# Kernel optimization log

Hardware: AMD Instinct MI355X
Metric: run time of the kernel (lower is better)

The kernel has to match this reference:

```python
import jax, jax.numpy as jnp
import numpy as np

NR_ACTIONS = 64
VEC_SIZE = 512
BATCH = 2048


def setup_inputs() -> dict:
    key = jax.random.key(0)
    k1, k2, k3 = jax.random.split(key, 3)
    v = jax.random.normal(k1, (BATCH, VEC_SIZE), dtype=jnp.float32)
    action = jax.random.randint(k2, (BATCH,), 0, NR_ACTIONS, dtype=jnp.int32)
    # nn.Linear(vec_size, vec_size) default init: U(-1/sqrt(in), 1/sqrt(in))
    bound = 1.0 / np.sqrt(VEC_SIZE)
    weights = jax.random.uniform(
        k3, (NR_ACTIONS, VEC_SIZE, VEC_SIZE), dtype=jnp.float32,
        minval=-bound, maxval=bound)
    return {"v": v, "action": action, "weights": weights}


def reference(v, action, weights):
    # pred[b] = v[b] @ weights[action[b]]  (row-vector times gathered matrix,
    # matching v.unsqueeze(1).bmm(weights.index_select(0, action)).squeeze(1))
    return jnp.einsum('bi,bij->bj', v, weights[action])
```

## Files before the change

kernel.cpp:

```cpp
#include <hip/hip_runtime.h>
#include <hip/hip_bf16.h>

#define NR_ACTIONS 64
#define VEC 512
#define MAXB 2048

typedef short bf16x8 __attribute__((ext_vector_type(8)));
typedef float f32x4  __attribute__((ext_vector_type(4)));

__device__ __forceinline__ uint32_t cvt2(float a, float b) {
    union { __hip_bfloat162 h; uint32_t u; } r;
    r.h = __float22bfloat162_rn(float2{a, b});
    return r.u;
}
__device__ __forceinline__ int aswz(int row, int kbyte) {
    return row * 1024 + (kbyte ^ ((row & 7) << 4));
}

__global__ __launch_bounds__(512) void half_gemm(
    const float* __restrict__ v, const int* __restrict__ action,
    const float* __restrict__ W, float* __restrict__ out, int batch)
{
    __shared__ __align__(16) char sA[16 * 1024];
    __shared__ ushort slist[MAXB];
    __shared__ int    smc;

    const int b    = blockIdx.x;
    const int a    = b & 63;
    const int half = b >> 6;
    const int tid  = threadIdx.x;
    const int lane = tid & 63;
    const int wv   = tid >> 6;
    const int li   = lane & 15;
    const int g    = lane >> 4;
    const int colg = half * 128 + wv * 16 + li;

    const float* Wa = W + (size_t)a * VEC * VEC;
    const bool fast = (batch == MAXB);

    if (wv == 0) {
        int m0 = 0;
        if (fast) {
            int av[32];
#pragma unroll
            for (int c = 0; c < 32; ++c) av[c] = action[c * 64 + lane];
#pragma unroll
            for (int c = 0; c < 32; ++c) {
                const bool hit = (av[c] == a);
                const unsigned long long mk = __ballot(hit);
                const int pos = m0 + __popcll(mk & ((1ull << lane) - 1ull));
                if (hit) slist[pos] = (ushort)(c * 64 + lane);
                m0 += __popcll(mk);
            }
        } else {
            for (int it = 0; it < batch; it += 64) {
                const int idx = it + lane;
                const bool hit = (idx < batch) && (action[idx] == a);
                const unsigned long long mk = __ballot(hit);
                const int pos = m0 + __popcll(mk & ((1ull << lane) - 1ull));
                if (hit && pos < MAXB) slist[pos] = (ushort)idx;
                m0 += __popcll(mk);
            }
        }
        if (lane == 0) smc = m0;
    }
    __syncthreads();
    const int m = smc;
    if (m == 0) return;

    const int arow = tid >> 5;
    const int akc  = tid & 31;

    float4 pA[4], pB[4];
    {
        const int ridx = slist[arow < m ? arow : 0];
        const float* ap = v + (size_t)ridx * VEC + akc * 16;
#pragma unroll
        for (int i = 0; i < 4; ++i) pA[i] = *(const float4*)(ap + i * 4);
    }

    bf16x8 Bf[16];
#pragma unroll
    for (int ks = 0; ks < 16; ++ks) {
        const float* wp = Wa + (size_t)(ks * 32 + g * 8) * VEC + colg;
        float t[8];
#pragma unroll
        for (int e = 0; e < 8; ++e) t[e] = wp[(size_t)e * VEC];
        union { uint32_t u[4]; bf16x8 s; } bu;
        bu.u[0] = cvt2(t[0], t[1]);
        bu.u[1] = cvt2(t[2], t[3]);
        bu.u[2] = cvt2(t[4], t[5]);
        bu.u[3] = cvt2(t[6], t[7]);
        Bf[ks] = bu.s;
    }

    int w0 = 0;
    while (true) {
        {
            uint4 p;
            p.x = cvt2(pA[0].x, pA[0].y); p.y = cvt2(pA[0].z, pA[0].w);
            p.z = cvt2(pA[1].x, pA[1].y); p.w = cvt2(pA[1].z, pA[1].w);
            *(uint4*)(sA + aswz(arow, akc * 32)) = p;
            p.x = cvt2(pA[2].x, pA[2].y); p.y = cvt2(pA[2].z, pA[2].w);
            p.z = cvt2(pA[3].x, pA[3].y); p.w = cvt2(pA[3].z, pA[3].w);
            *(uint4*)(sA + aswz(arow, akc * 32 + 16)) = p;
        }
        __syncthreads();

        if (w0 + 16 < m) {
            const int rl = w0 + 16 + arow;
            const int ridx = slist[rl < m ? rl : 0];
            const float* ap = v + (size_t)ridx * VEC + akc * 16;
#pragma unroll
            for (int i = 0; i < 4; ++i) pB[i] = *(const float4*)(ap + i * 4);
        }

        f32x4 acc = {0.f, 0.f, 0.f, 0.f};
#pragma unroll
        for (int ks = 0; ks < 16; ++ks) {
            const bf16x8 af = *(const bf16x8*)(sA + aswz(li, ks * 64 + g * 16));
            acc = __builtin_amdgcn_mfma_f32_16x16x32_bf16(af, Bf[ks], acc, 0, 0, 0);
        }
#pragma unroll
        for (int q = 0; q < 4; ++q) {
            const int row = w0 + g * 4 + q;
            if (row < m)
                out[(size_t)slist[row] * VEC + colg] = acc[q];
        }

        w0 += 16;
        if (w0 >= m) break;
        __syncthreads();
#pragma unroll
        for (int i = 0; i < 4; ++i) pA[i] = pB[i];
    }
}

__global__ void naive_vm(const float* __restrict__ v, const float* __restrict__ W,
                         const int* __restrict__ action, float* __restrict__ out) {
    const int b = blockIdx.x;
    const int a = action[b];
    const float* wbase = W + (size_t)a * VEC * VEC;
    const float* vb = v + (size_t)b * VEC;
    const int j = threadIdx.x;
    float acc0 = 0.f, acc1 = 0.f;
    for (int k = 0; k < VEC; ++k) {
        const float vk = vb[k];
        acc0 = fmaf(vk, wbase[(size_t)k * VEC + j], acc0);
        acc1 = fmaf(vk, wbase[(size_t)k * VEC + j + 256], acc1);
    }
    out[(size_t)b * VEC + j] = acc0;
    out[(size_t)b * VEC + j + 256] = acc1;
}

extern "C" void kernel_launch(void* const* d_in, const int* in_sizes, int n_in,
                              void* d_out, int out_size, void* d_ws, size_t ws_size,
                              hipStream_t stream) {
    const float* v      = (const float*)d_in[0];
    const int*   action = (const int*)d_in[1];
    const float* W      = (const float*)d_in[2];
    float* out = (float*)d_out;
    const int batch = in_sizes[1];
    if (batch <= 0) return;

    if (batch > MAXB) {
        naive_vm<<<batch, 256, 0, stream>>>(v, W, action, out);
        return;
    }
    half_gemm<<<NR_ACTIONS * 4, 512, 0, stream>>>(v, action, W, out, batch);
}
```

Baseline: 20.94 us.

## Stage up to 48 gathered rows per block before loading weights

The kernel now gathers and converts up to 48 selected input rows into shared memory in a single stage, before the weight fragments are loaded, instead of double-buffering 16-row tiles. The goal is to overlap the input gather latency with the weight loads and to cut the per-tile barriers for the common case of about 32 rows per action. The shared-memory A buffer grows threefold, which may reduce occupancy, and batches with more than 48 rows per action fall back to a loop without prefetch.

```diff
diff --git a/kernel.cpp b/kernel.cpp
--- a/kernel.cpp
+++ b/kernel.cpp
@@ -4,6 +4,7 @@
 #define NR_ACTIONS 64
 #define VEC 512
 #define MAXB 2048
+#define WROWS 48
 
 typedef short bf16x8 __attribute__((ext_vector_type(8)));
 typedef float f32x4  __attribute__((ext_vector_type(4)));
@@ -17,11 +18,11 @@
     return row * 1024 + (kbyte ^ ((row & 7) << 4));
 }
 
-__global__ __launch_bounds__(512) void half_gemm(
+__global__ __launch_bounds__(512) void half_gemm48(
     const float* __restrict__ v, const int* __restrict__ action,
     const float* __restrict__ W, float* __restrict__ out, int batch)
 {
-    __shared__ __align__(16) char sA[16 * 1024];
+    __shared__ __align__(16) char sA[WROWS * 1024];
     __shared__ ushort slist[MAXB];
     __shared__ int    smc;
 
@@ -71,12 +72,23 @@
     const int arow = tid >> 5;
     const int akc  = tid & 31;
 
-    float4 pA[4], pB[4];
-    {
-        const int ridx = slist[arow < m ? arow : 0];
-        const float* ap = v + (size_t)ridx * VEC + akc * 16;
-#pragma unroll
-        for (int i = 0; i < 4; ++i) pA[i] = *(const float4*)(ap + i * 4);
+#pragma unroll
+    for (int j = 0; j < 3; ++j) {
+        const int row = arow + 16 * j;
+        if (row < m && row < WROWS) {
+            const float* ap = v + (size_t)slist[row] * VEC + akc * 16;
+            const float4 p0 = *(const float4*)(ap);
+            const float4 p1 = *(const float4*)(ap + 4);
+            const float4 p2 = *(const float4*)(ap + 8);
+            const float4 p3 = *(const float4*)(ap + 12);
+            uint4 q;
+            q.x = cvt2(p0.x, p0.y); q.y = cvt2(p0.z, p0.w);
+            q.z = cvt2(p1.x, p1.y); q.w = cvt2(p1.z, p1.w);
+            *(uint4*)(sA + aswz(row, akc * 32)) = q;
+            q.x = cvt2(p2.x, p2.y); q.y = cvt2(p2.z, p2.w);
+            q.z = cvt2(p3.x, p3.y); q.w = cvt2(p3.z, p3.w);
+            *(uint4*)(sA + aswz(row, akc * 32 + 16)) = q;
+        }
     }
 
     bf16x8 Bf[16];
@@ -94,45 +106,80 @@
         Bf[ks] = bu.s;
     }
 
-    int w0 = 0;
-    while (true) {
-        {
-            uint4 p;
-            p.x = cvt2(pA[0].x, pA[0].y); p.y = cvt2(pA[0].z, pA[0].w);
-            p.z = cvt2(pA[1].x, pA[1].y); p.w = cvt2(pA[1].z, pA[1].w);
-            *(uint4*)(sA + aswz(arow, akc * 32)) = p;
-            p.x = cvt2(pA[2].x, pA[2].y); p.y = cvt2(pA[2].z, pA[2].w);
-            p.z = cvt2(pA[3].x, pA[3].y); p.w = cvt2(pA[3].z, pA[3].w);
-            *(uint4*)(sA + aswz(arow, akc * 32 + 16)) = p;
-        }
+    __syncthreads();
+
+    f32x4 acc0 = {0.f, 0.f, 0.f, 0.f};
+#pragma unroll
+    for (int ks = 0; ks < 16; ++ks) {
+        const bf16x8 af = *(const bf16x8*)(sA + aswz(li, ks * 64 + g * 16));
+        acc0 = __builtin_amdgcn_mfma_f32_16x16x32_bf16(af, Bf[ks], acc0, 0, 0, 0);
+    }
+    f32x4 acc1 = {0.f, 0.f, 0.f, 0.f};
+    if (m > 16) {
+#pragma unroll
+        for (int ks = 0; ks < 16; ++ks) {
+            const bf16x8 af = *(const bf16x8*)(sA + aswz(16 + li, ks * 64 + g * 16));
+            acc1 = __builtin_amdgcn_mfma_f32_16x16x32_bf16(af, Bf[ks], acc1, 0, 0, 0);
+        }
+    }
+    f32x4 acc2 = {0.f, 0.f, 0.f, 0.f};
+    if (m > 32) {
+#pragma unroll
+        for (int ks = 0; ks < 16; ++ks) {
+            const bf16x8 af = *(const bf16x8*)(sA + aswz(32 + li, ks * 64 + g * 16));
+            acc2 = __builtin_amdgcn_mfma_f32_16x16x32_bf16(af, Bf[ks], acc2, 0, 0, 0);
+        }
+    }
+
+#pragma unroll
+    for (int q = 0; q < 4; ++q) {
+        const int r0 = g * 4 + q;
+        if (r0 < m) out[(size_t)slist[r0] * VEC + colg] = acc0[q];
+        const int r1 = 16 + g * 4 + q;
+        if (r1 < m) out[(size_t)slist[r1] * VEC + colg] = acc1[q];
+        const int r2 = 32 + g * 4 + q;
+        if (r2 < m && r2 < WROWS) out[(size_t)slist[r2] * VEC + colg] = acc2[q];
+    }
+
+    for (int w0 = WROWS; w0 < m; w0 += WROWS) {
         __syncthreads();
-
-        if (w0 + 16 < m) {
-            const int rl = w0 + 16 + arow;
-            const int ridx = slist[rl < m ? rl : 0];
-            const float* ap = v + (size_t)ridx * VEC + akc * 16;
-#pragma unroll
-            for (int i = 0; i < 4; ++i) pB[i] = *(const float4*)(ap + i * 4);
-        }
-
-        f32x4 acc = {0.f, 0.f, 0.f, 0.f};
-#pragma unroll
-        for (int ks = 0; ks < 16; ++ks) {
-            const bf16x8 af = *(const bf16x8*)(sA + aswz(li, ks * 64 + g * 16));
-            acc = __builtin_amdgcn_mfma_f32_16x16x32_bf16(af, Bf[ks], acc, 0, 0, 0);
-        }
-#pragma unroll
-        for (int q = 0; q < 4; ++q) {
-            const int row = w0 + g * 4 + q;
-            if (row < m)
-                out[(size_t)slist[row] * VEC + colg] = acc[q];
-        }
-
-        w0 += 16;
-        if (w0 >= m) break;
+#pragma unroll
+        for (int j = 0; j < 3; ++j) {
+            const int row = arow + 16 * j;
+            if (w0 + row < m && row < WROWS) {
+                const float* ap = v + (size_t)slist[w0 + row] * VEC + akc * 16;
+                const float4 p0 = *(const float4*)(ap);
+                const float4 p1 = *(const float4*)(ap + 4);
+                const float4 p2 = *(const float4*)(ap + 8);
+                const float4 p3 = *(const float4*)(ap + 12);
+                uint4 q;
+                q.x = cvt2(p0.x, p0.y); q.y = cvt2(p0.z, p0.w);
+                q.z = cvt2(p1.x, p1.y); q.w = cvt2(p1.z, p1.w);
+                *(uint4*)(sA + aswz(row, akc * 32)) = q;
+                q.x = cvt2(p2.x, p2.y); q.y = cvt2(p2.z, p2.w);
+                q.z = cvt2(p3.x, p3.y); q.w = cvt2(p3.z, p3.w);
+                *(uint4*)(sA + aswz(row, akc * 32 + 16)) = q;
+            }
+        }
         __syncthreads();
 #pragma unroll
-        for (int i = 0; i < 4; ++i) pA[i] = pB[i];
+        for (int rb = 0; rb < 3; ++rb) {
+            if (w0 + rb * 16 < m) {
+                f32x4 acc = {0.f, 0.f, 0.f, 0.f};
+#pragma unroll
+                for (int ks = 0; ks < 16; ++ks) {
+                    const bf16x8 af =
+                        *(const bf16x8*)(sA + aswz(rb * 16 + li, ks * 64 + g * 16));
+                    acc = __builtin_amdgcn_mfma_f32_16x16x32_bf16(af, Bf[ks], acc, 0, 0, 0);
+                }
+#pragma unroll
+                for (int q = 0; q < 4; ++q) {
+                    const int rr = w0 + rb * 16 + g * 4 + q;
+                    if (rr < m && rb * 16 + g * 4 + q < WROWS)
+                        out[(size_t)slist[rr] * VEC + colg] = acc[q];
+                }
+            }
+        }
     }
 }
 
@@ -167,5 +214,5 @@
         naive_vm<<<batch, 256, 0, stream>>>(v, W, action, out);
         return;
     }
-    half_gemm<<<NR_ACTIONS * 4, 512, 0, stream>>>(v, action, W, out, batch);
-}
+    half_gemm48<<<NR_ACTIONS * 4, 512, 0, stream>>>(v, action, W, out, batch);
+}
```

Result: no change. 20.60 us (-1.6%).
